# Kernel tuning notes

Measured on AMD Instinct MI355X. Metric: run time of the kernel, lower is better.

Reference implementation:

```python
import jax, jax.numpy as jnp
import numpy as np

IN_F = 4096
OUT_F = 4096
N_TOK = 8192  # batch 4 * seq 2048 tokens


def setup_inputs() -> dict:
    key = jax.random.key(0)
    k1, k2, k3 = jax.random.split(key, 3)
    x = jax.random.normal(k1, (N_TOK, IN_F), dtype=jnp.float16)
    # int4-range quantized weights stored as int8, as produced by quantize_weight()
    weight_q = jax.random.randint(k2, (OUT_F, IN_F), -8, 8, dtype=jnp.int8)
    # positive per-output-channel scales (weight_max/7, clamped >= 1e-5)
    weight_scale = (jax.random.uniform(k3, (OUT_F,), dtype=jnp.float32) * 0.01 + 1e-4).astype(jnp.float16)
    return {"x": x, "weight_q": weight_q, "weight_scale": weight_scale}


def reference(x, weight_q, weight_scale):
    # per-token symmetric int4 activation quantization
    x_max = jnp.max(jnp.abs(x), axis=-1, keepdims=True)          # [N, 1]
    x_scale = jnp.maximum(x_max / jnp.float16(7.0), jnp.float16(1e-5))
    x_q = jnp.clip(jnp.round(x / x_scale), -8, 7)                # int4 values in fp16
    # fp32 GEMM emulating int4xint4 matmul
    acc = jnp.matmul(x_q.astype(jnp.float32), weight_q.astype(jnp.float32).T)  # [N, OUT]
    # dequant: (x_scale * weight_scale) is [N, OUT]; unsqueeze(0) as in original
    scale = (x_scale.astype(jnp.float32) * weight_scale.astype(jnp.float32)[None, :])[None]  # [1, N, OUT]
    out = acc * scale                                            # [1, N, OUT]
    return out.astype(x.dtype)
```

## Files before the change

kernel.cpp:

```cpp
#include <hip/hip_runtime.h>
#include <hip/hip_fp16.h>
#include <stdint.h>

#define K_DIM 4096
#define N_OUT 4096
#define BM 256
#define BN 128
#define BKB 64

typedef __attribute__((ext_vector_type(4))) int int32x4;
typedef __attribute__((ext_vector_type(16))) int int32x16;

__global__ __launch_bounds__(256) void quant_x(const float* __restrict__ x,
                                               int8_t* __restrict__ xq,
                                               float* __restrict__ xs) {
  const int row = blockIdx.x;
  const int t = threadIdx.x;
  const float4* xr = (const float4*)(x + (size_t)row * K_DIM);
  float4 v[4];
  float m = 0.f;
#pragma unroll
  for (int i = 0; i < 4; ++i) {
    v[i] = xr[t * 4 + i];
    m = fmaxf(m, fmaxf(fmaxf(fabsf(v[i].x), fabsf(v[i].y)),
                       fmaxf(fabsf(v[i].z), fabsf(v[i].w))));
  }
#pragma unroll
  for (int off = 32; off > 0; off >>= 1) m = fmaxf(m, __shfl_xor(m, off));
  __shared__ float wmax[4];
  if ((t & 63) == 0) wmax[t >> 6] = m;
  __syncthreads();
  m = fmaxf(fmaxf(wmax[0], wmax[1]), fmaxf(wmax[2], wmax[3]));

  const float eps = 1.0013580322265625e-05f;
  const float xscale = fmaxf(m / 7.0f, eps);
  if (t == 0) xs[row] = xscale;

  uint32_t p[4];
#pragma unroll
  for (int g = 0; g < 4; ++g) {
    const float* fv = (const float*)&v[g];
    uint32_t w = 0;
#pragma unroll
    for (int j = 0; j < 4; ++j) {
      float r = rintf(fv[j] / xscale);
      r = fminf(fmaxf(r, -8.f), 7.f);
      w |= ((uint32_t)(uint8_t)(int8_t)(int)r) << (8 * j);
    }
    p[g] = w;
  }
  *(uint4*)(xq + (size_t)row * K_DIM + t * 16) = *(uint4*)p;
}

__global__ __launch_bounds__(256) void pack_w(const int* __restrict__ w,
                                              uint32_t* __restrict__ wqf) {
  const int c = blockIdx.x * 256 + threadIdx.x;
  const int blk = c >> 6;
  const int l = c & 63;
  const int row = ((blk >> 7) << 5) + (l & 31);
  const int k = ((blk & 127) << 5) + ((l >> 5) << 4);
  const int4* src = (const int4*)(w + (size_t)row * K_DIM + k);
  uint32_t p[4];
#pragma unroll
  for (int g = 0; g < 4; ++g) {
    const int4 v = src[g];
    p[g] = (uint32_t)(v.x & 255) | ((uint32_t)(v.y & 255) << 8) |
           ((uint32_t)(v.z & 255) << 16) | ((uint32_t)(v.w & 255) << 24);
  }
  *(uint4*)(wqf + (size_t)c * 4) = *(uint4*)p;
}

__global__ __launch_bounds__(512, 4) void gemm_w4a4(
    const int8_t* __restrict__ xq, const uint8_t* __restrict__ wqf,
    const float* __restrict__ xs, const float* __restrict__ wscale,
    float* __restrict__ out, int M) {
  __shared__ uint8_t lds[2][24576];

  const int bid = blockIdx.x;
  const int xcd = bid & 7;
  const int i_loc = bid >> 3;
  const int mt = xcd * 4 + (i_loc & 3);
  const int nt = i_loc >> 2;
  const int tm = mt * BM;
  const int tn = nt * BN;

  const int t = threadIdx.x;
  const int l = t & 63;
  const int wv = t >> 6;
  const int wm = wv >> 1;
  const int wn = wv & 1;

  const uint8_t* gAw = (const uint8_t*)xq +
                       (size_t)(tm + wv * 32 + (l & 31)) * K_DIM +
                       ((l >> 5) << 4);
  const uint8_t* gBw = wqf +
                       ((size_t)(nt * 4 + (wv >> 1)) * 128 + (wv & 1)) * 1024 +
                       (size_t)l * 16;

  int32x16 acc[2][2] = {};

  auto stage = [&](int buf, int sg) {
    const int ktb = (sg & 63) * BKB;
#pragma unroll
    for (int j = 0; j < 2; ++j) {
      __builtin_amdgcn_global_load_lds(
          (const __attribute__((address_space(1))) uint32_t*)(gAw + ktb + j * 32),
          (__attribute__((address_space(3))) uint32_t*)(
              &lds[buf][(wv * 2 + j) * 1024 + l * 16]),
          16, 0, 0);
    }
    __builtin_amdgcn_global_load_lds(
        (const __attribute__((address_space(1))) uint32_t*)(
            gBw + (size_t)(sg & 63) * 2048),
        (__attribute__((address_space(3))) uint32_t*)(
            &lds[buf][16384 + wv * 1024 + l * 16]),
        16, 0, 0);
  };

  const int nsteps = K_DIM / BKB;

  stage(0, 0);
  asm volatile("s_waitcnt vmcnt(0)" ::: "memory");
  __builtin_amdgcn_s_barrier();

  for (int s = 0; s < nsteps; ++s) {
    const int buf = s & 1;
    stage(buf ^ 1, s + 1);

    const uint8_t* aB = &lds[buf][wm * 4096 + l * 16];
    const uint8_t* bB = &lds[buf][16384 + wn * 4096 + l * 16];
    int32x4 a0[2], a1[2], b0[2], b1[2];
#pragma unroll
    for (int i = 0; i < 2; ++i) {
      a0[i] = *(const int32x4*)(aB + i * 2048);
      b0[i] = *(const int32x4*)(bB + i * 2048);
      a1[i] = *(const int32x4*)(aB + i * 2048 + 1024);
      b1[i] = *(const int32x4*)(bB + i * 2048 + 1024);
    }
#pragma unroll
    for (int i = 0; i < 2; ++i)
#pragma unroll
      for (int j = 0; j < 2; ++j)
        acc[i][j] = __builtin_amdgcn_mfma_i32_32x32x32_i8(a0[i], b0[j],
                                                          acc[i][j], 0, 0, 0);
#pragma unroll
    for (int i = 0; i < 2; ++i)
#pragma unroll
      for (int j = 0; j < 2; ++j)
        acc[i][j] = __builtin_amdgcn_mfma_i32_32x32x32_i8(a1[i], b1[j],
                                                          acc[i][j], 0, 0, 0);

    asm volatile("s_waitcnt vmcnt(0)" ::: "memory");
    __builtin_amdgcn_s_barrier();
  }

  const int colbase = tn + wn * 64;
  const int rowbase = tm + wm * 64 + 4 * (l >> 5);
#pragma unroll
  for (int m = 0; m < 2; ++m) {
#pragma unroll
    for (int n = 0; n < 2; ++n) {
      const int col = colbase + n * 32 + (l & 31);
      const float wsc = wscale[col];
#pragma unroll
      for (int j = 0; j < 16; ++j) {
        const int row = rowbase + m * 32 + (j & 3) + 8 * (j >> 2);
        const float val = (float)acc[m][n][j] * (xs[row] * wsc);
        out[(size_t)row * N_OUT + col] = __half2float(__float2half(val));
      }
    }
  }
}

extern "C" void kernel_launch(void* const* d_in, const int* in_sizes, int n_in,
                              void* d_out, int out_size, void* d_ws, size_t ws_size,
                              hipStream_t stream) {
  const float* x = (const float*)d_in[0];
  const int* w = (const int*)d_in[1];
  const float* wsc = (const float*)d_in[2];
  float* out = (float*)d_out;

  const int M = in_sizes[0] / K_DIM;

  uint8_t* ws = (uint8_t*)d_ws;
  int8_t* xq = (int8_t*)ws;
  uint8_t* wqf = ws + (size_t)M * K_DIM;
  float* xs = (float*)(ws + (size_t)M * K_DIM + (size_t)N_OUT * K_DIM);

  quant_x<<<M, 256, 0, stream>>>(x, xq, xs);
  pack_w<<<(N_OUT * K_DIM / 16) / 256, 256, 0, stream>>>(w, (uint32_t*)wqf);
  gemm_w4a4<<<(M / BM) * (N_OUT / BN), 512, 0, stream>>>(
      xq, wqf, xs, wsc, out, M);
}
```

Before: 224.5 us.

## Enlarge GEMM tile to 256x256 with triple-buffered LDS and phased MFMA schedule

Doubles the N tile to 256 so each wave computes a 128x64 output block (8 accumulators), raising arithmetic intensity per loaded byte. The LDS ring grows from two to three buffers, and loads are issued two stages ahead with partial vmcnt waits. Each K-step is split into two MFMA phases, each bracketed by a barrier and raised wave priority, with the A and B global loads spread across the phases. In exchange it doubles accumulator registers and LDS use, drops occupancy to two blocks per CU, and halves the grid size, which could leave CUs underused.

```diff
diff --git a/kernel.cpp b/kernel.cpp
--- a/kernel.cpp
+++ b/kernel.cpp
@@ -5,7 +5,7 @@
 #define K_DIM 4096
 #define N_OUT 4096
 #define BM 256
-#define BN 128
+#define BN 256
 #define BKB 64
 
 typedef __attribute__((ext_vector_type(4))) int int32x4;
@@ -70,11 +70,11 @@
   *(uint4*)(wqf + (size_t)c * 4) = *(uint4*)p;
 }
 
-__global__ __launch_bounds__(512, 4) void gemm_w4a4(
+__global__ __launch_bounds__(512, 2) void gemm_w4a4(
     const int8_t* __restrict__ xq, const uint8_t* __restrict__ wqf,
     const float* __restrict__ xs, const float* __restrict__ wscale,
     float* __restrict__ out, int M) {
-  __shared__ uint8_t lds[2][24576];
+  __shared__ uint8_t lds[3][32768];
 
   const int bid = blockIdx.x;
   const int xcd = bid & 7;
@@ -87,77 +87,117 @@
   const int t = threadIdx.x;
   const int l = t & 63;
   const int wv = t >> 6;
-  const int wm = wv >> 1;
-  const int wn = wv & 1;
-
-  const uint8_t* gAw = (const uint8_t*)xq +
-                       (size_t)(tm + wv * 32 + (l & 31)) * K_DIM +
-                       ((l >> 5) << 4);
-  const uint8_t* gBw = wqf +
-                       ((size_t)(nt * 4 + (wv >> 1)) * 128 + (wv & 1)) * 1024 +
-                       (size_t)l * 16;
-
-  int32x16 acc[2][2] = {};
-
-  auto stage = [&](int buf, int sg) {
-    const int ktb = (sg & 63) * BKB;
+  const int wm = wv >> 2;
+  const int wn = wv & 3;
+
+  const uint8_t* gA = (const uint8_t*)xq +
+                      (size_t)(tm + wv * 32 + (l & 31)) * K_DIM +
+                      ((l >> 5) << 4);
+  const uint8_t* gB = wqf + (size_t)(nt * 8 + wv) * 131072 + (size_t)l * 16;
+
+  int32x16 acc[4][2] = {};
+
+  auto stageA2 = [&](int buf, int ss) {
 #pragma unroll
     for (int j = 0; j < 2; ++j) {
       __builtin_amdgcn_global_load_lds(
-          (const __attribute__((address_space(1))) uint32_t*)(gAw + ktb + j * 32),
+          (const __attribute__((address_space(1))) uint32_t*)(
+              gA + ss * BKB + j * 32),
           (__attribute__((address_space(3))) uint32_t*)(
               &lds[buf][(wv * 2 + j) * 1024 + l * 16]),
           16, 0, 0);
     }
-    __builtin_amdgcn_global_load_lds(
-        (const __attribute__((address_space(1))) uint32_t*)(
-            gBw + (size_t)(sg & 63) * 2048),
-        (__attribute__((address_space(3))) uint32_t*)(
-            &lds[buf][16384 + wv * 1024 + l * 16]),
-        16, 0, 0);
   };
+  auto stageB2 = [&](int buf, int ss) {
+#pragma unroll
+    for (int j = 0; j < 2; ++j) {
+      __builtin_amdgcn_global_load_lds(
+          (const __attribute__((address_space(1))) uint32_t*)(
+              gB + ((size_t)(ss * 2 + j) << 10)),
+          (__attribute__((address_space(3))) uint32_t*)(
+              &lds[buf][16384 + (wv * 2 + j) * 1024 + l * 16]),
+          16, 0, 0);
+    }
+  };
+
+#define PHASE_OPEN()                                    \
+  __builtin_amdgcn_s_barrier();                         \
+  asm volatile("s_waitcnt lgkmcnt(0)" ::: "memory");    \
+  __builtin_amdgcn_sched_barrier(0);                    \
+  __builtin_amdgcn_s_setprio(1);
+
+#define PHASE_CLOSE()                                   \
+  __builtin_amdgcn_s_setprio(0);
 
   const int nsteps = K_DIM / BKB;
 
-  stage(0, 0);
+  stageA2(0, 0);
+  stageB2(0, 0);
+  stageA2(1, 1);
+  stageB2(1, 1);
+  asm volatile("s_waitcnt vmcnt(4)" ::: "memory");
+  __builtin_amdgcn_s_barrier();
+
+  for (int s = 0; s < nsteps; ++s) {
+    const int buf = s % 3;
+    const int sbuf = (s + 2) % 3;
+    const int ss = (s + 2) & 63;
+    const uint8_t* aB = &lds[buf][(wm * 4) * 2048 + l * 16];
+    const uint8_t* bB = &lds[buf][16384 + (wn * 2) * 2048 + l * 16];
+
+    int32x4 a[2][2], b[2][2];
+#pragma unroll
+    for (int m = 0; m < 2; ++m)
+#pragma unroll
+      for (int ks = 0; ks < 2; ++ks)
+        a[m][ks] = *(const int32x4*)(aB + m * 2048 + ks * 1024);
+#pragma unroll
+    for (int n = 0; n < 2; ++n)
+#pragma unroll
+      for (int ks = 0; ks < 2; ++ks)
+        b[n][ks] = *(const int32x4*)(bB + n * 2048 + ks * 1024);
+    stageA2(sbuf, ss);
+    PHASE_OPEN()
+#pragma unroll
+    for (int ks = 0; ks < 2; ++ks)
+#pragma unroll
+      for (int m = 0; m < 2; ++m)
+#pragma unroll
+        for (int n = 0; n < 2; ++n)
+          acc[m][n] = __builtin_amdgcn_mfma_i32_32x32x32_i8(
+              a[m][ks], b[n][ks], acc[m][n], 0, 0, 0);
+    PHASE_CLOSE()
+    __builtin_amdgcn_s_barrier();
+
+    int32x4 c[2][2];
+#pragma unroll
+    for (int m = 0; m < 2; ++m)
+#pragma unroll
+      for (int ks = 0; ks < 2; ++ks)
+        c[m][ks] = *(const int32x4*)(aB + (2 + m) * 2048 + ks * 1024);
+    stageB2(sbuf, ss);
+    PHASE_OPEN()
+#pragma unroll
+    for (int ks = 0; ks < 2; ++ks)
+#pragma unroll
+      for (int m = 0; m < 2; ++m)
+#pragma unroll
+        for (int n = 0; n < 2; ++n)
+          acc[2 + m][n] = __builtin_amdgcn_mfma_i32_32x32x32_i8(
+              c[m][ks], b[n][ks], acc[2 + m][n], 0, 0, 0);
+    PHASE_CLOSE()
+    asm volatile("s_waitcnt vmcnt(4)" ::: "memory");
+    __builtin_amdgcn_s_barrier();
+  }
   asm volatile("s_waitcnt vmcnt(0)" ::: "memory");
-  __builtin_amdgcn_s_barrier();
-
-  for (int s = 0; s < nsteps; ++s) {
-    const int buf = s & 1;
-    stage(buf ^ 1, s + 1);
-
-    const uint8_t* aB = &lds[buf][wm * 4096 + l * 16];
-    const uint8_t* bB = &lds[buf][16384 + wn * 4096 + l * 16];
-    int32x4 a0[2], a1[2], b0[2], b1[2];
-#pragma unroll
-    for (int i = 0; i < 2; ++i) {
-      a0[i] = *(const int32x4*)(aB + i * 2048);
-      b0[i] = *(const int32x4*)(bB + i * 2048);
-      a1[i] = *(const int32x4*)(aB + i * 2048 + 1024);
-      b1[i] = *(const int32x4*)(bB + i * 2048 + 1024);
-    }
-#pragma unroll
-    for (int i = 0; i < 2; ++i)
-#pragma unroll
-      for (int j = 0; j < 2; ++j)
-        acc[i][j] = __builtin_amdgcn_mfma_i32_32x32x32_i8(a0[i], b0[j],
-                                                          acc[i][j], 0, 0, 0);
-#pragma unroll
-    for (int i = 0; i < 2; ++i)
-#pragma unroll
-      for (int j = 0; j < 2; ++j)
-        acc[i][j] = __builtin_amdgcn_mfma_i32_32x32x32_i8(a1[i], b1[j],
-                                                          acc[i][j], 0, 0, 0);
-
-    asm volatile("s_waitcnt vmcnt(0)" ::: "memory");
-    __builtin_amdgcn_s_barrier();
-  }
+
+#undef PHASE_OPEN
+#undef PHASE_CLOSE
 
   const int colbase = tn + wn * 64;
-  const int rowbase = tm + wm * 64 + 4 * (l >> 5);
-#pragma unroll
-  for (int m = 0; m < 2; ++m) {
+  const int rowbase = tm + wm * 128 + 4 * (l >> 5);
+#pragma unroll
+  for (int m = 0; m < 4; ++m) {
 #pragma unroll
     for (int n = 0; n < 2; ++n) {
       const int col = colbase + n * 32 + (l & 31);
```

New measurement: 194.4 us (median of 2 runs). 13.4% less time.
